# Optimization experiments

Measured on AMD Instinct MI355X. Metric: run time of the kernel, lower is better.

## Reference

```python
import jax, jax.numpy as jnp
import numpy as np

N = 100000   # nodes
E = 1600000  # edges
D = 128      # input = hidden channels
L = 4        # 1 + num_convs GIN layers
G = 512      # graphs in batch
BN_EPS = 1e-5


def setup_inputs() -> dict:
    key = jax.random.key(0)
    ks = jax.random.split(key, 10)
    s = 1.0 / np.sqrt(D)
    x = jax.random.normal(ks[0], (N, D), jnp.float32)
    edge_index = jax.random.randint(ks[1], (2, E), 0, N)
    batch = jnp.sort(jax.random.randint(ks[2], (N,), 0, G))
    return {
        "x": x,
        "edge_index": edge_index,
        "batch": batch,
        "W1": jax.random.normal(ks[3], (L, D, D), jnp.float32) * s,
        "b1": jnp.zeros((L, D), jnp.float32),
        "gamma": jnp.ones((L, D), jnp.float32),
        "beta": jnp.zeros((L, D), jnp.float32),
        "W2": jax.random.normal(ks[4], (L, D, D), jnp.float32) * s,
        "b2": jnp.zeros((L, D), jnp.float32),
        "lin_W": jax.random.normal(ks[5], (D, 2), jnp.float32) * s,
        "lin_b": jnp.zeros((2,), jnp.float32),
    }


def reference(x, edge_index, batch, W1, b1, gamma, beta, W2, b2, lin_W, lin_b):
    src, dst = edge_index[0], edge_index[1]
    h = x
    for l in range(L):
        # GINConv, eps=0: (1+eps)*x_i + sum_{j->i} x_j  (scatter-add over edges)
        agg = jax.ops.segment_sum(h[src], dst, num_segments=N)  # [N, D]
        z = h + agg
        # MLP: Linear -> BatchNorm1d (training stats) -> ELU -> Linear -> ELU
        z = z @ W1[l] + b1[l]
        mu = jnp.mean(z, axis=0)
        var = jnp.mean((z - mu) ** 2, axis=0)  # biased var, as torch BN
        z = (z - mu) * jax.lax.rsqrt(var + BN_EPS) * gamma[l] + beta[l]
        z = jax.nn.elu(z)
        h = jax.nn.elu(z @ W2[l] + b2[l])
    # global_mean_pool: per-graph segment mean
    sums = jax.ops.segment_sum(h, batch, num_segments=G)             # [G, D]
    cnt = jax.ops.segment_sum(jnp.ones((N, 1), h.dtype), batch, num_segments=G)
    pooled = sums / jnp.maximum(cnt, 1.0)
    return pooled @ lin_W + lin_b  # [G, 2]
```

## Files before the change

### kernel.cpp

```cpp
#include <hip/hip_runtime.h>
#include <cstdint>

#define D 128
#define BKT_SHIFT 8
#define BKT_CAP 5120
#define EDGES_PER_BLOCK 4096
#define NREP 8
#define LCAP 1536

typedef __attribute__((ext_vector_type(4))) float floatx4;
typedef __attribute__((ext_vector_type(4))) _Float16 half4;
typedef __attribute__((ext_vector_type(8))) _Float16 half8;

__device__ __forceinline__ float elu_f(float x) {
    return x > 0.0f ? x : __expf(x) - 1.0f;
}

__global__ __launch_bounds__(256) void bucket_scatter_kernel(
    const int* __restrict__ src, const int* __restrict__ dst,
    int* __restrict__ gcursor, int2* __restrict__ staging, int E, int NB) {
    __shared__ int lcnt[512];
    __shared__ int lbase[512];
    int t = threadIdx.x;
    lcnt[t] = 0; lcnt[t + 256] = 0;
    __syncthreads();
    int base = blockIdx.x * EDGES_PER_BLOCK;
    int s_[16], d_[16], r_[16];
#pragma unroll
    for (int i = 0; i < 16; ++i) {
        int idx = base + i * 256 + t;
        if (idx < E) {
            s_[i] = src[idx];
            d_[i] = dst[idx];
            r_[i] = atomicAdd(&lcnt[d_[i] >> BKT_SHIFT], 1);
        }
    }
    __syncthreads();
    for (int b = t; b < NB; b += 256) {
        int c = lcnt[b];
        if (c) lbase[b] = atomicAdd(&gcursor[b], c);
    }
    __syncthreads();
#pragma unroll
    for (int i = 0; i < 16; ++i) {
        int idx = base + i * 256 + t;
        if (idx < E) {
            int bkt = d_[i] >> BKT_SHIFT;
            staging[lbase[bkt] + r_[i]] = make_int2(s_[i], d_[i]);
        }
    }
}

__global__ __launch_bounds__(256) void bucket_build_kernel(
    const int2* __restrict__ staging, const int* __restrict__ gcursor,
    int* __restrict__ rowstart, int* __restrict__ rowend,
    int* __restrict__ col, int N) {
    __shared__ int hcnt[256];
    __shared__ int hoff[256];
    int t = threadIdx.x;
    int node0 = blockIdx.x << BKT_SHIFT;
    int off0 = blockIdx.x * BKT_CAP;
    int off1 = gcursor[blockIdx.x];
    hcnt[t] = 0;
    __syncthreads();
    for (int i = off0 + t; i < off1; i += 256)
        atomicAdd(&hcnt[staging[i].y - node0], 1);
    __syncthreads();
    int deg = hcnt[t];
    hoff[t] = deg;
    __syncthreads();
    for (int off = 1; off < 256; off <<= 1) {
        int u = (t >= off) ? hoff[t - off] : 0;
        __syncthreads();
        hoff[t] += u;
        __syncthreads();
    }
    int myoff = (t == 0) ? 0 : hoff[t - 1];
    __syncthreads();
    hoff[t] = myoff;
    hcnt[t] = 0;
    if (node0 + t < N) {
        rowstart[node0 + t] = off0 + myoff;
        rowend[node0 + t] = off0 + myoff + deg;
    }
    __syncthreads();
    for (int i = off0 + t; i < off1; i += 256) {
        int2 p = staging[i];
        int dl = p.y - node0;
        int pos = off0 + hoff[dl] + atomicAdd(&hcnt[dl], 1);
        col[pos] = p.x;
    }
}

__global__ __launch_bounds__(256) void prep_kernel(
    const float* __restrict__ x, _Float16* __restrict__ hhalf, int n4,
    const float* __restrict__ W1, const float* __restrict__ W2,
    _Float16* __restrict__ Wph, _Float16* __restrict__ Wpl, int wtot,
    int* __restrict__ gcursor, int NB, int nbh, int nbw) {
    int bid = blockIdx.x;
    int t = threadIdx.x;
    if (bid < nbh) {
        int i = bid * 256 + t;
        if (i >= n4) return;
        float4 v = ((const float4*)x)[i];
        half4 h = {(_Float16)v.x, (_Float16)v.y, (_Float16)v.z, (_Float16)v.w};
        ((half4*)hhalf)[i] = h;
    } else if (bid < nbh + nbw) {
        int idx = (bid - nbh) * 256 + t;
        if (idx >= wtot) return;
        int mat = idx >> 14;
        int rem = idx & 16383;
        int tile = rem >> 9;
        int lane = (rem >> 3) & 63;
        int j = rem & 7;
        int ks = tile >> 3, nt = tile & 7;
        int n = nt * 16 + (lane & 15);
        int k = ks * 32 + (lane >> 4) * 8 + j;
        int l = mat >> 1;
        const float* W = (mat & 1) ? W2 : W1;
        float v = W[(size_t)l * D * D + k * D + n];
        _Float16 h = (_Float16)v;
        _Float16 lo = (_Float16)(v - (float)h);
        Wph[idx] = h;
        Wpl[idx] = lo;
    } else {
        int i = (bid - nbh - nbw) * 256 + t;
        if (i < NB) gcursor[i] = i * BKT_CAP;
    }
}

template <bool GATHER, bool ELU_OUT, bool STATS, bool POOL, int MW>
__global__ __launch_bounds__(256, MW) void gemm_mfma(
    const _Float16* __restrict__ Hh,
    const int* __restrict__ rowstart, const int* __restrict__ rowend,
    const int* __restrict__ col,
    const _Float16* __restrict__ Z,
    const _Float16* __restrict__ Wph, const _Float16* __restrict__ Wpl,
    const float* __restrict__ bias,
    const float* __restrict__ colsum_in, const float* __restrict__ gamma,
    const float* __restrict__ beta,
    _Float16* __restrict__ outp16, float* __restrict__ colsum_out,
    const int* __restrict__ batchg, float* __restrict__ pooled, float* __restrict__ cnt,
    int N) {
    __shared__ _Float16 sA[64 * 136];
    __shared__ float bnsum[2 * D];
    __shared__ float s_sc[D];
    __shared__ float s_sh[D];
    __shared__ int lcol[LCAP];
    __shared__ int srow[65];
    const int tid = threadIdx.x;
    const int row0 = blockIdx.x * 64;

    if (STATS && tid < 2 * D) bnsum[tid] = 0.f;

    if (GATHER) {
        const int lastrow = (row0 + 63 < N) ? row0 + 63 : N - 1;
        const int eb0 = rowstart[row0];
        const int eb1 = rowend[lastrow];
        if (tid < 64) {
            int rr = row0 + tid;
            srow[tid] = (rr < N) ? rowstart[rr] : eb1;
        }
        if (tid == 64) srow[64] = eb1;
        for (int k = eb0 + tid; k < eb1 && (k - eb0) < LCAP; k += 256)
            lcol[k - eb0] = col[k];
        __syncthreads();

        const int rg = tid >> 4;
        const int q = tid & 15;
        const half8* hh8 = (const half8*)Hh;
#define LIDX(ee) ((((ee) - eb0) < LCAP) ? lcol[(ee) - eb0] : col[(ee)])
#pragma unroll
        for (int i = 0; i < 4; ++i) {
            int r = rg * 4 + i;
            int node = row0 + r;
            float a0 = 0.f, a1 = 0.f, a2 = 0.f, a3 = 0.f;
            float a4 = 0.f, a5 = 0.f, a6 = 0.f, a7 = 0.f;
            if (node < N) {
                half8 sf = hh8[(uint32_t)(node * 16 + q)];
                a0 = (float)sf[0]; a1 = (float)sf[1]; a2 = (float)sf[2]; a3 = (float)sf[3];
                a4 = (float)sf[4]; a5 = (float)sf[5]; a6 = (float)sf[6]; a7 = (float)sf[7];
                int e0 = srow[r], e1 = srow[r + 1];
                int e = e0;
                for (; e + 15 < e1; e += 16) {
                    int j0 = LIDX(e),      j1 = LIDX(e + 1),  j2 = LIDX(e + 2),  j3 = LIDX(e + 3);
                    int j4 = LIDX(e + 4),  j5 = LIDX(e + 5),  j6 = LIDX(e + 6),  j7 = LIDX(e + 7);
                    int j8 = LIDX(e + 8),  j9 = LIDX(e + 9),  jA = LIDX(e + 10), jB = LIDX(e + 11);
                    int jC = LIDX(e + 12), jD = LIDX(e + 13), jE = LIDX(e + 14), jF = LIDX(e + 15);
                    half8 v0 = hh8[(uint32_t)(j0 * 16 + q)];
                    half8 v1 = hh8[(uint32_t)(j1 * 16 + q)];
                    half8 v2 = hh8[(uint32_t)(j2 * 16 + q)];
                    half8 v3 = hh8[(uint32_t)(j3 * 16 + q)];
                    half8 v4 = hh8[(uint32_t)(j4 * 16 + q)];
                    half8 v5 = hh8[(uint32_t)(j5 * 16 + q)];
                    half8 v6 = hh8[(uint32_t)(j6 * 16 + q)];
                    half8 v7 = hh8[(uint32_t)(j7 * 16 + q)];
                    half8 v8 = hh8[(uint32_t)(j8 * 16 + q)];
                    half8 v9 = hh8[(uint32_t)(j9 * 16 + q)];
                    half8 vA = hh8[(uint32_t)(jA * 16 + q)];
                    half8 vB = hh8[(uint32_t)(jB * 16 + q)];
                    half8 vC = hh8[(uint32_t)(jC * 16 + q)];
                    half8 vD = hh8[(uint32_t)(jD * 16 + q)];
                    half8 vE = hh8[(uint32_t)(jE * 16 + q)];
                    half8 vF = hh8[(uint32_t)(jF * 16 + q)];
#pragma unroll
                    for (int c = 0; c < 8; ++c) {
                        float s = (((float)v0[c] + (float)v1[c]) + ((float)v2[c] + (float)v3[c]))
                                + (((float)v4[c] + (float)v5[c]) + ((float)v6[c] + (float)v7[c]))
                                + (((float)v8[c] + (float)v9[c]) + ((float)vA[c] + (float)vB[c]))
                                + (((float)vC[c] + (float)vD[c]) + ((float)vE[c] + (float)vF[c]));
                        if (c == 0) a0 += s; else if (c == 1) a1 += s;
                        else if (c == 2) a2 += s; else if (c == 3) a3 += s;
                        else if (c == 4) a4 += s; else if (c == 5) a5 += s;
                        else if (c == 6) a6 += s; else a7 += s;
                    }
                }
                if (e + 7 < e1) {
                    int j0 = LIDX(e),     j1 = LIDX(e + 1), j2 = LIDX(e + 2), j3 = LIDX(e + 3);
                    int j4 = LIDX(e + 4), j5 = LIDX(e + 5), j6 = LIDX(e + 6), j7 = LIDX(e + 7);
                    half8 v0 = hh8[(uint32_t)(j0 * 16 + q)];
                    half8 v1 = hh8[(uint32_t)(j1 * 16 + q)];
                    half8 v2 = hh8[(uint32_t)(j2 * 16 + q)];
                    half8 v3 = hh8[(uint32_t)(j3 * 16 + q)];
                    half8 v4 = hh8[(uint32_t)(j4 * 16 + q)];
                    half8 v5 = hh8[(uint32_t)(j5 * 16 + q)];
                    half8 v6 = hh8[(uint32_t)(j6 * 16 + q)];
                    half8 v7 = hh8[(uint32_t)(j7 * 16 + q)];
                    a0 += (((float)v0[0] + (float)v1[0]) + ((float)v2[0] + (float)v3[0]))
                        + (((float)v4[0] + (float)v5[0]) + ((float)v6[0] + (float)v7[0]));
                    a1 += (((float)v0[1] + (float)v1[1]) + ((float)v2[1] + (float)v3[1]))
                        + (((float)v4[1] + (float)v5[1]) + ((float)v6[1] + (float)v7[1]));
                    a2 += (((float)v0[2] + (float)v1[2]) + ((float)v2[2] + (float)v3[2]))
                        + (((float)v4[2] + (float)v5[2]) + ((float)v6[2] + (float)v7[2]));
                    a3 += (((float)v0[3] + (float)v1[3]) + ((float)v2[3] + (float)v3[3]))
                        + (((float)v4[3] + (float)v5[3]) + ((float)v6[3] + (float)v7[3]));
                    a4 += (((float)v0[4] + (float)v1[4]) + ((float)v2[4] + (float)v3[4]))
                        + (((float)v4[4] + (float)v5[4]) + ((float)v6[4] + (float)v7[4]));
                    a5 += (((float)v0[5] + (float)v1[5]) + ((float)v2[5] + (float)v3[5]))
                        + (((float)v4[5] + (float)v5[5]) + ((float)v6[5] + (float)v7[5]));
                    a6 += (((float)v0[6] + (float)v1[6]) + ((float)v2[6] + (float)v3[6]))
                        + (((float)v4[6] + (float)v5[6]) + ((float)v6[6] + (float)v7[6]));
                    a7 += (((float)v0[7] + (float)v1[7]) + ((float)v2[7] + (float)v3[7]))
                        + (((float)v4[7] + (float)v5[7]) + ((float)v6[7] + (float)v7[7]));
                    e += 8;
                }
                if (e < e1) {
                    int last = e1 - 1;
                    int e0c = e,     e1c = e + 1 > last ? last : e + 1;
                    int e2c = e + 2 > last ? last : e + 2, e3c = e + 3 > last ? last : e + 3;
                    int e4c = e + 4 > last ? last : e + 4, e5c = e + 5 > last ? last : e + 5;
                    int e6c = e + 6 > last ? last : e + 6, e7c = e + 7 > last ? last : e + 7;
                    int j0 = LIDX(e0c), j1 = LIDX(e1c), j2 = LIDX(e2c), j3 = LIDX(e3c);
                    int j4 = LIDX(e4c), j5 = LIDX(e5c), j6 = LIDX(e6c), j7 = LIDX(e7c);
                    float m1 = (e + 1 <= last) ? 1.f : 0.f, m2 = (e + 2 <= last) ? 1.f : 0.f;
                    float m3 = (e + 3 <= last) ? 1.f : 0.f, m4 = (e + 4 <= last) ? 1.f : 0.f;
                    float m5 = (e + 5 <= last) ? 1.f : 0.f, m6 = (e + 6 <= last) ? 1.f : 0.f;
                    float m7 = (e + 7 <= last) ? 1.f : 0.f;
                    half8 v0 = hh8[(uint32_t)(j0 * 16 + q)];
                    half8 v1 = hh8[(uint32_t)(j1 * 16 + q)];
                    half8 v2 = hh8[(uint32_t)(j2 * 16 + q)];
                    half8 v3 = hh8[(uint32_t)(j3 * 16 + q)];
                    half8 v4 = hh8[(uint32_t)(j4 * 16 + q)];
                    half8 v5 = hh8[(uint32_t)(j5 * 16 + q)];
                    half8 v6 = hh8[(uint32_t)(j6 * 16 + q)];
                    half8 v7 = hh8[(uint32_t)(j7 * 16 + q)];
                    a0 += (float)v0[0] + m1 * (float)v1[0] + m2 * (float)v2[0] + m3 * (float)v3[0]
                        + m4 * (float)v4[0] + m5 * (float)v5[0] + m6 * (float)v6[0] + m7 * (float)v7[0];
                    a1 += (float)v0[1] + m1 * (float)v1[1] + m2 * (float)v2[1] + m3 * (float)v3[1]
                        + m4 * (float)v4[1] + m5 * (float)v5[1] + m6 * (float)v6[1] + m7 * (float)v7[1];
                    a2 += (float)v0[2] + m1 * (float)v1[2] + m2 * (float)v2[2] + m3 * (float)v3[2]
                        + m4 * (float)v4[2] + m5 * (float)v5[2] + m6 * (float)v6[2] + m7 * (float)v7[2];
                    a3 += (float)v0[3] + m1 * (float)v1[3] + m2 * (float)v2[3] + m3 * (float)v3[3]
                        + m4 * (float)v4[3] + m5 * (float)v5[3] + m6 * (float)v6[3] + m7 * (float)v7[3];
                    a4 += (float)v0[4] + m1 * (float)v1[4] + m2 * (float)v2[4] + m3 * (float)v3[4]
                        + m4 * (float)v4[4] + m5 * (float)v5[4] + m6 * (float)v6[4] + m7 * (float)v7[4];
                    a5 += (float)v0[5] + m1 * (float)v1[5] + m2 * (float)v2[5] + m3 * (float)v3[5]
                        + m4 * (float)v4[5] + m5 * (float)v5[5] + m6 * (float)v6[5] + m7 * (float)v7[5];
                    a6 += (float)v0[6] + m1 * (float)v1[6] + m2 * (float)v2[6] + m3 * (float)v3[6]
                        + m4 * (float)v4[6] + m5 * (float)v5[6] + m6 * (float)v6[6] + m7 * (float)v7[6];
                    a7 += (float)v0[7] + m1 * (float)v1[7] + m2 * (float)v2[7] + m3 * (float)v3[7]
                        + m4 * (float)v4[7] + m5 * (float)v5[7] + m6 * (float)v6[7] + m7 * (float)v7[7];
                }
            }
            half8 hv = {(_Float16)a0, (_Float16)a1, (_Float16)a2, (_Float16)a3,
                        (_Float16)a4, (_Float16)a5, (_Float16)a6, (_Float16)a7};
            *(half8*)&sA[r * 136 + q * 8] = hv;
        }
#undef LIDX
    } else {
        if (tid < D) {
            float s = 0.f, s2 = 0.f;
#pragma unroll
            for (int rp = 0; rp < NREP; ++rp) {
                s  += colsum_in[rp * 2 * D + tid];
                s2 += colsum_in[rp * 2 * D + D + tid];
            }
            float invN = 1.0f / (float)N;
            float mu = s * invN;
            float var = s2 * invN - mu * mu;
            float rs = rsqrtf(var + 1e-5f);
            float sc = gamma[tid] * rs;
            s_sc[tid] = sc;
            s_sh[tid] = beta[tid] - mu * sc;
        }
        __syncthreads();
#pragma unroll
        for (int it = 0; it < 4; ++it) {
            int idx = tid + it * 256;
            int r = idx >> 4;
            int q8 = (idx & 15) * 8;
            int gr = row0 + r;
            half8 z = {};
            if (gr < N) z = *(const half8*)&Z[(size_t)gr * D + q8];
            float v0 = elu_f((float)z[0] * s_sc[q8 + 0] + s_sh[q8 + 0]);
            float v1 = elu_f((float)z[1] * s_sc[q8 + 1] + s_sh[q8 + 1]);
            float v2 = elu_f((float)z[2] * s_sc[q8 + 2] + s_sh[q8 + 2]);
            float v3 = elu_f((float)z[3] * s_sc[q8 + 3] + s_sh[q8 + 3]);
            float v4 = elu_f((float)z[4] * s_sc[q8 + 4] + s_sh[q8 + 4]);
            float v5 = elu_f((float)z[5] * s_sc[q8 + 5] + s_sh[q8 + 5]);
            float v6 = elu_f((float)z[6] * s_sc[q8 + 6] + s_sh[q8 + 6]);
            float v7 = elu_f((float)z[7] * s_sc[q8 + 7] + s_sh[q8 + 7]);
            half8 hv = {(_Float16)v0, (_Float16)v1, (_Float16)v2, (_Float16)v3,
                        (_Float16)v4, (_Float16)v5, (_Float16)v6, (_Float16)v7};
            *(half8*)&sA[r * 136 + q8] = hv;
        }
    }
    __syncthreads();

    const int wave = tid >> 6, lane = tid & 63;
    const int wm = wave >> 1, wn = wave & 1;
    const int l15 = lane & 15, quad = lane >> 4;
    const half8* bph = (const half8*)Wph;
    const half8* bpl = (const half8*)Wpl;

    floatx4 acc[2][4];
#pragma unroll
    for (int mt = 0; mt < 2; ++mt)
#pragma unroll
        for (int nt = 0; nt < 4; ++nt)
            acc[mt][nt] = (floatx4){0.f, 0.f, 0.f, 0.f};

#pragma unroll
    for (int ks = 0; ks < 4; ++ks) {
        const int kf = ks * 32 + quad * 8;
        half8 ah[2];
#pragma unroll
        for (int mt = 0; mt < 2; ++mt)
            ah[mt] = *(const half8*)&sA[(wm * 32 + mt * 16 + l15) * 136 + kf];
#pragma unroll
        for (int nt = 0; nt < 4; ++nt) {
            int tIdx = (ks * 8 + wn * 4 + nt) * 64 + lane;
            half8 bh = bph[tIdx];
            half8 bl = bpl[tIdx];
            acc[0][nt] = __builtin_amdgcn_mfma_f32_16x16x32_f16(ah[0], bh, acc[0][nt], 0, 0, 0);
            acc[1][nt] = __builtin_amdgcn_mfma_f32_16x16x32_f16(ah[1], bh, acc[1][nt], 0, 0, 0);
            acc[0][nt] = __builtin_amdgcn_mfma_f32_16x16x32_f16(ah[0], bl, acc[0][nt], 0, 0, 0);
            acc[1][nt] = __builtin_amdgcn_mfma_f32_16x16x32_f16(ah[1], bl, acc[1][nt], 0, 0, 0);
        }
    }

    int* sbatch = (int*)s_sc;
    if (POOL) {
        if (tid < 64) {
            int rr = row0 + tid;
            sbatch[tid] = (rr < N) ? batchg[rr] : -1;
        }
        __syncthreads();
    }

#pragma unroll
    for (int nt = 0; nt < 4; ++nt) {
        int c = wn * 64 + nt * 16 + l15;
        float b = bias[c];
        float s = 0.f, s2 = 0.f;
#pragma unroll
        for (int mt = 0; mt < 2; ++mt) {
#pragma unroll
            for (int r = 0; r < 4; ++r) {
                int rl = wm * 32 + mt * 16 + quad * 4 + r;
                int gm = row0 + rl;
                float v = acc[mt][nt][r] + b;
                if (ELU_OUT) v = elu_f(v);
                if (POOL) {
                    if (gm < N) sA[rl * 136 + c] = (_Float16)v;
                } else if (gm < N) {
                    outp16[(size_t)gm * D + c] = (_Float16)v;
                    if (STATS) { s += v; s2 += v * v; }
                }
            }
        }
        if (STATS) {
            atomicAdd(&bnsum[c], s);
            atomicAdd(&bnsum[D + c], s2);
        }
    }
    if (STATS) {
        __syncthreads();
        float* rep = colsum_out + (size_t)(blockIdx.x & (NREP - 1)) * 2 * D;
        if (tid < D) {
            atomicAdd(&rep[tid], bnsum[tid]);
            atomicAdd(&rep[D + tid], bnsum[D + tid]);
        }
    }
    if (POOL) {
        __syncthreads();
        int c = tid & 127, half = tid >> 7;
        int rb = half * 32;
        int cur = -1; float pacc = 0.f; float cc = 0.f;
        for (int i = 0; i < 32; ++i) {
            int r = rb + i;
            int gm = row0 + r;
            if (gm >= N) break;
            int g = sbatch[r];
            if (g != cur) {
                if (cur >= 0) {
                    atomicAdd(&pooled[(size_t)cur * D + c], pacc);
                    if (c == 0) atomicAdd(&cnt[cur], cc);
                }
                cur = g; pacc = 0.f; cc = 0.f;
            }
            pacc += (float)sA[r * 136 + c];
            cc += 1.f;
        }
        if (cur >= 0) {
            atomicAdd(&pooled[(size_t)cur * D + c], pacc);
            if (c == 0) atomicAdd(&cnt[cur], cc);
        }
    }
}

__global__ void final_linear_kernel(const float* __restrict__ pooled,
                                    const float* __restrict__ cnt,
                                    const float* __restrict__ linW,
                                    const float* __restrict__ linb,
                                    float* __restrict__ out, int G) {
    int t = blockIdx.x * blockDim.x + threadIdx.x;
    if (t >= G * 2) return;
    int g = t >> 1, o = t & 1;
    float inv = 1.0f / fmaxf(cnt[g], 1.0f);
    float s = linb[o];
    for (int c = 0; c < D; ++c)
        s += pooled[(size_t)g * D + c] * inv * linW[c * 2 + o];
    out[t] = s;
}

extern "C" void kernel_launch(void* const* d_in, const int* in_sizes, int n_in,
                              void* d_out, int out_size, void* d_ws, size_t ws_size,
                              hipStream_t stream) {
    const float* x      = (const float*)d_in[0];
    const int*  eidx    = (const int*)d_in[1];
    const int*  batch   = (const int*)d_in[2];
    const float* W1     = (const float*)d_in[3];
    const float* b1     = (const float*)d_in[4];
    const float* gamma  = (const float*)d_in[5];
    const float* beta   = (const float*)d_in[6];
    const float* W2     = (const float*)d_in[7];
    const float* b2     = (const float*)d_in[8];
    const float* linW   = (const float*)d_in[9];
    const float* linb   = (const float*)d_in[10];
    float* out = (float*)d_out;

    const int N = in_sizes[0] / D;
    const int E = in_sizes[1] / 2;
    const int L = in_sizes[3] / (D * D);
    const int G = out_size / 2;
    const int* esrc = eidx;
    const int* edst = eidx + E;
    const int NB = (N + 255) >> 8;

    size_t off = 0;
    auto carve = [&](size_t bytes) -> void* {
        void* p = (char*)d_ws + off;
        off += (bytes + 255) & ~(size_t)255;
        return p;
    };
    const size_t ND = (size_t)N * D;
    const int WTOT = 2 * L * D * D;
    _Float16* z16   = (_Float16*)carve(ND * 2);
    _Float16* hhalf = (_Float16*)carve(ND * 2);
    _Float16* Wph = (_Float16*)carve((size_t)WTOT * 2);
    _Float16* Wpl = (_Float16*)carve((size_t)WTOT * 2);
    int* rowstart = (int*)carve((size_t)N * 4);
    int* rowend   = (int*)carve((size_t)N * 4);
    int* col      = (int*)carve((size_t)NB * BKT_CAP * 4);
    const size_t cs_bytes = ((size_t)4 * NREP * 2 * D * 4 + 255) & ~(size_t)255;
    const size_t pl_bytes = ((size_t)G * D * 4 + 255) & ~(size_t)255;
    float* colsum4 = (float*)carve((size_t)4 * NREP * 2 * D * 4);
    float* pooled  = (float*)carve((size_t)G * D * 4);
    float* cnt     = (float*)carve((size_t)G * 4);
    int* gcursor   = (int*)carve(512 * 4);
    int2* staging = (int2*)z16;
    (void)ws_size; (void)n_in;

    hipMemsetAsync(colsum4, 0, cs_bytes + pl_bytes + (size_t)G * 4, stream);

    const int EB = (E + EDGES_PER_BLOCK - 1) / EDGES_PER_BLOCK;
    const int n4 = (int)(ND / 4);
    const int nbh = (n4 + 255) / 256;
    const int nbw = (WTOT + 255) / 256;
    const int nbc = (NB + 255) / 256;
    prep_kernel<<<nbh + nbw + nbc, 256, 0, stream>>>(
        x, hhalf, n4, W1, W2, Wph, Wpl, WTOT, gcursor, NB, nbh, nbw);
    bucket_scatter_kernel<<<EB, 256, 0, stream>>>(esrc, edst, gcursor, staging, E, NB);
    bucket_build_kernel<<<NB, 256, 0, stream>>>(staging, gcursor, rowstart, rowend, col, N);

    const int gemm_grid = (N + 63) / 64;
    for (int l = 0; l < L; ++l) {
        float* colsum = colsum4 + (size_t)l * NREP * 2 * D;
        gemm_mfma<true, false, true, false, 4><<<gemm_grid, 256, 0, stream>>>(
            hhalf, rowstart, rowend, col, nullptr,
            Wph + (size_t)(l * 2) * D * D, Wpl + (size_t)(l * 2) * D * D,
            b1 + (size_t)l * D, nullptr, nullptr, nullptr, z16, colsum,
            nullptr, nullptr, nullptr, N);
        if (l < L - 1) {
            gemm_mfma<false, true, false, false, 8><<<gemm_grid, 256, 0, stream>>>(
                nullptr, nullptr, nullptr, nullptr, z16,
                Wph + (size_t)(l * 2 + 1) * D * D, Wpl + (size_t)(l * 2 + 1) * D * D,
                b2 + (size_t)l * D, colsum, gamma + (size_t)l * D, beta + (size_t)l * D,
                hhalf, nullptr, nullptr, nullptr, nullptr, N);
        } else {
            gemm_mfma<false, true, false, true, 8><<<gemm_grid, 256, 0, stream>>>(
                nullptr, nullptr, nullptr, nullptr, z16,
                Wph + (size_t)(l * 2 + 1) * D * D, Wpl + (size_t)(l * 2 + 1) * D * D,
                b2 + (size_t)l * D, colsum, gamma + (size_t)l * D, beta + (size_t)l * D,
                nullptr, nullptr, batch, pooled, cnt, N);
        }
    }

    final_linear_kernel<<<(G * 2 + 255) / 256, 256, 0, stream>>>(pooled, cnt, linW, linb, out, G);
}
```

Baseline: 588.7 us.

## Split aggregation into feature-sliced gather kernel with sliced node layout

Node features are now stored in a column-sliced layout (8 slices of 16 halves per node), and neighbor aggregation moves out of the first GEMM into a separate kernel. Each block of that kernel handles one slice for 64 rows, so each slice's working set (about 3.2 MB) is more likely to stay in cache across the random gathers. The first GEMM then reads the sliced aggregate, and the second GEMM writes sliced output. The cost is an extra kernel launch per layer, an extra write and read of the aggregate array, an eightfold reread of the column indices, and strided stores in the sliced output.

```diff
diff --git a/kernel.cpp b/kernel.cpp
--- a/kernel.cpp
+++ b/kernel.cpp
@@ -93,7 +93,7 @@
 }
 
 __global__ __launch_bounds__(256) void prep_kernel(
-    const float* __restrict__ x, _Float16* __restrict__ hhalf, int n4,
+    const float* __restrict__ x, _Float16* __restrict__ hsl, int n4, int N,
     const float* __restrict__ W1, const float* __restrict__ W2,
     _Float16* __restrict__ Wph, _Float16* __restrict__ Wpl, int wtot,
     int* __restrict__ gcursor, int NB, int nbh, int nbw) {
@@ -104,7 +104,10 @@
         if (i >= n4) return;
         float4 v = ((const float4*)x)[i];
         half4 h = {(_Float16)v.x, (_Float16)v.y, (_Float16)v.z, (_Float16)v.w};
-        ((half4*)hhalf)[i] = h;
+        int nrow = i >> 5;
+        int c4 = (i & 31) * 4;
+        int sl = c4 >> 4, cin = c4 & 15;
+        *(half4*)(hsl + ((size_t)sl * N + nrow) * 16 + cin) = h;
     } else if (bid < nbh + nbw) {
         int idx = (bid - nbh) * 256 + t;
         if (idx >= wtot) return;
@@ -129,12 +132,132 @@
     }
 }
 
-template <bool GATHER, bool ELU_OUT, bool STATS, bool POOL, int MW>
-__global__ __launch_bounds__(256, MW) void gemm_mfma(
-    const _Float16* __restrict__ Hh,
+__global__ __launch_bounds__(256) void agg_slice_kernel(
+    const _Float16* __restrict__ hsl,
     const int* __restrict__ rowstart, const int* __restrict__ rowend,
     const int* __restrict__ col,
-    const _Float16* __restrict__ Z,
+    _Float16* __restrict__ aggsl, int N) {
+    __shared__ int lcol[LCAP];
+    __shared__ int srow[65];
+    __shared__ float pf[64][2][8];
+    const int tid = threadIdx.x;
+    const int s = blockIdx.x & 7;
+    const int row0 = (blockIdx.x >> 3) * 64;
+    const int lastrow = (row0 + 63 < N) ? row0 + 63 : N - 1;
+    const int eb0 = rowstart[row0];
+    const int eb1 = rowend[lastrow];
+    if (tid < 64) {
+        int rr = row0 + tid;
+        srow[tid] = (rr < N) ? rowstart[rr] : eb1;
+    }
+    if (tid == 64) srow[64] = eb1;
+    for (int k = eb0 + tid; k < eb1 && (k - eb0) < LCAP; k += 256)
+        lcol[k - eb0] = __builtin_nontemporal_load(&col[k]);
+    __syncthreads();
+
+    const int q2 = tid & 1;
+    const int g  = (tid >> 1) & 1;
+    const int r  = tid >> 2;
+    const int node = row0 + r;
+    const _Float16* hb = hsl + (size_t)s * N * 16;
+    float a0 = 0.f, a1 = 0.f, a2 = 0.f, a3 = 0.f;
+    float a4 = 0.f, a5 = 0.f, a6 = 0.f, a7 = 0.f;
+#define LIDX(ee) ((((ee) - eb0) < LCAP) ? lcol[(ee) - eb0] : col[(ee)])
+    if (node < N) {
+        int e1 = srow[r + 1];
+        int e = srow[r] + g;
+        for (; e + 14 < e1; e += 16) {
+            int j0 = LIDX(e),      j1 = LIDX(e + 2),  j2 = LIDX(e + 4),  j3 = LIDX(e + 6);
+            int j4 = LIDX(e + 8),  j5 = LIDX(e + 10), j6 = LIDX(e + 12), j7 = LIDX(e + 14);
+            half8 v0 = *(const half8*)(hb + (uint32_t)j0 * 16 + q2 * 8);
+            half8 v1 = *(const half8*)(hb + (uint32_t)j1 * 16 + q2 * 8);
+            half8 v2 = *(const half8*)(hb + (uint32_t)j2 * 16 + q2 * 8);
+            half8 v3 = *(const half8*)(hb + (uint32_t)j3 * 16 + q2 * 8);
+            half8 v4 = *(const half8*)(hb + (uint32_t)j4 * 16 + q2 * 8);
+            half8 v5 = *(const half8*)(hb + (uint32_t)j5 * 16 + q2 * 8);
+            half8 v6 = *(const half8*)(hb + (uint32_t)j6 * 16 + q2 * 8);
+            half8 v7 = *(const half8*)(hb + (uint32_t)j7 * 16 + q2 * 8);
+            a0 += (((float)v0[0] + (float)v1[0]) + ((float)v2[0] + (float)v3[0]))
+                + (((float)v4[0] + (float)v5[0]) + ((float)v6[0] + (float)v7[0]));
+            a1 += (((float)v0[1] + (float)v1[1]) + ((float)v2[1] + (float)v3[1]))
+                + (((float)v4[1] + (float)v5[1]) + ((float)v6[1] + (float)v7[1]));
+            a2 += (((float)v0[2] + (float)v1[2]) + ((float)v2[2] + (float)v3[2]))
+                + (((float)v4[2] + (float)v5[2]) + ((float)v6[2] + (float)v7[2]));
+            a3 += (((float)v0[3] + (float)v1[3]) + ((float)v2[3] + (float)v3[3]))
+                + (((float)v4[3] + (float)v5[3]) + ((float)v6[3] + (float)v7[3]));
+            a4 += (((float)v0[4] + (float)v1[4]) + ((float)v2[4] + (float)v3[4]))
+                + (((float)v4[4] + (float)v5[4]) + ((float)v6[4] + (float)v7[4]));
+            a5 += (((float)v0[5] + (float)v1[5]) + ((float)v2[5] + (float)v3[5]))
+                + (((float)v4[5] + (float)v5[5]) + ((float)v6[5] + (float)v7[5]));
+            a6 += (((float)v0[6] + (float)v1[6]) + ((float)v2[6] + (float)v3[6]))
+                + (((float)v4[6] + (float)v5[6]) + ((float)v6[6] + (float)v7[6]));
+            a7 += (((float)v0[7] + (float)v1[7]) + ((float)v2[7] + (float)v3[7]))
+                + (((float)v4[7] + (float)v5[7]) + ((float)v6[7] + (float)v7[7]));
+        }
+        if (e < e1) {
+            int last = e1 - 1;
+            int e0c = e;
+            int e1c = e + 2  > last ? last : e + 2,  e2c = e + 4  > last ? last : e + 4;
+            int e3c = e + 6  > last ? last : e + 6,  e4c = e + 8  > last ? last : e + 8;
+            int e5c = e + 10 > last ? last : e + 10, e6c = e + 12 > last ? last : e + 12;
+            int e7c = e + 14 > last ? last : e + 14;
+            float m1 = (e + 2  <= last) ? 1.f : 0.f, m2 = (e + 4  <= last) ? 1.f : 0.f;
+            float m3 = (e + 6  <= last) ? 1.f : 0.f, m4 = (e + 8  <= last) ? 1.f : 0.f;
+            float m5 = (e + 10 <= last) ? 1.f : 0.f, m6 = (e + 12 <= last) ? 1.f : 0.f;
+            float m7 = (e + 14 <= last) ? 1.f : 0.f;
+            int j0 = LIDX(e0c), j1 = LIDX(e1c), j2 = LIDX(e2c), j3 = LIDX(e3c);
+            int j4 = LIDX(e4c), j5 = LIDX(e5c), j6 = LIDX(e6c), j7 = LIDX(e7c);
+            half8 v0 = *(const half8*)(hb + (uint32_t)j0 * 16 + q2 * 8);
+            half8 v1 = *(const half8*)(hb + (uint32_t)j1 * 16 + q2 * 8);
+            half8 v2 = *(const half8*)(hb + (uint32_t)j2 * 16 + q2 * 8);
+            half8 v3 = *(const half8*)(hb + (uint32_t)j3 * 16 + q2 * 8);
+            half8 v4 = *(const half8*)(hb + (uint32_t)j4 * 16 + q2 * 8);
+            half8 v5 = *(const half8*)(hb + (uint32_t)j5 * 16 + q2 * 8);
+            half8 v6 = *(const half8*)(hb + (uint32_t)j6 * 16 + q2 * 8);
+            half8 v7 = *(const half8*)(hb + (uint32_t)j7 * 16 + q2 * 8);
+            a0 += (float)v0[0] + m1 * (float)v1[0] + m2 * (float)v2[0] + m3 * (float)v3[0]
+                + m4 * (float)v4[0] + m5 * (float)v5[0] + m6 * (float)v6[0] + m7 * (float)v7[0];
+            a1 += (float)v0[1] + m1 * (float)v1[1] + m2 * (float)v2[1] + m3 * (float)v3[1]
+                + m4 * (float)v4[1] + m5 * (float)v5[1] + m6 * (float)v6[1] + m7 * (float)v7[1];
+            a2 += (float)v0[2] + m1 * (float)v1[2] + m2 * (float)v2[2] + m3 * (float)v3[2]
+                + m4 * (float)v4[2] + m5 * (float)v5[2] + m6 * (float)v6[2] + m7 * (float)v7[2];
+            a3 += (float)v0[3] + m1 * (float)v1[3] + m2 * (float)v2[3] + m3 * (float)v3[3]
+                + m4 * (float)v4[3] + m5 * (float)v5[3] + m6 * (float)v6[3] + m7 * (float)v7[3];
+            a4 += (float)v0[4] + m1 * (float)v1[4] + m2 * (float)v2[4] + m3 * (float)v3[4]
+                + m4 * (float)v4[4] + m5 * (float)v5[4] + m6 * (float)v6[4] + m7 * (float)v7[4];
+            a5 += (float)v0[5] + m1 * (float)v1[5] + m2 * (float)v2[5] + m3 * (float)v3[5]
+                + m4 * (float)v4[5] + m5 * (float)v5[5] + m6 * (float)v6[5] + m7 * (float)v7[5];
+            a6 += (float)v0[6] + m1 * (float)v1[6] + m2 * (float)v2[6] + m3 * (float)v3[6]
+                + m4 * (float)v4[6] + m5 * (float)v5[6] + m6 * (float)v6[6] + m7 * (float)v7[6];
+            a7 += (float)v0[7] + m1 * (float)v1[7] + m2 * (float)v2[7] + m3 * (float)v3[7]
+                + m4 * (float)v4[7] + m5 * (float)v5[7] + m6 * (float)v6[7] + m7 * (float)v7[7];
+        }
+    }
+#undef LIDX
+    if (g == 1) {
+        pf[r][q2][0] = a0; pf[r][q2][1] = a1; pf[r][q2][2] = a2; pf[r][q2][3] = a3;
+        pf[r][q2][4] = a4; pf[r][q2][5] = a5; pf[r][q2][6] = a6; pf[r][q2][7] = a7;
+    }
+    __syncthreads();
+    if (g == 0 && node < N) {
+        half8 sf = *(const half8*)(hb + (uint32_t)node * 16 + q2 * 8);
+        a0 += (float)sf[0] + pf[r][q2][0];
+        a1 += (float)sf[1] + pf[r][q2][1];
+        a2 += (float)sf[2] + pf[r][q2][2];
+        a3 += (float)sf[3] + pf[r][q2][3];
+        a4 += (float)sf[4] + pf[r][q2][4];
+        a5 += (float)sf[5] + pf[r][q2][5];
+        a6 += (float)sf[6] + pf[r][q2][6];
+        a7 += (float)sf[7] + pf[r][q2][7];
+        half8 hv = {(_Float16)a0, (_Float16)a1, (_Float16)a2, (_Float16)a3,
+                    (_Float16)a4, (_Float16)a5, (_Float16)a6, (_Float16)a7};
+        __builtin_nontemporal_store(hv, (half8*)(aggsl + ((size_t)s * N + node) * 16 + q2 * 8));
+    }
+}
+
+template <bool SLICED_IN, bool ELU_OUT, bool STATS, bool POOL, bool SLICED_OUT>
+__global__ __launch_bounds__(256, 8) void gemm_mfma(
+    const _Float16* __restrict__ Ain,
     const _Float16* __restrict__ Wph, const _Float16* __restrict__ Wpl,
     const float* __restrict__ bias,
     const float* __restrict__ colsum_in, const float* __restrict__ gamma,
@@ -146,147 +269,23 @@
     __shared__ float bnsum[2 * D];
     __shared__ float s_sc[D];
     __shared__ float s_sh[D];
-    __shared__ int lcol[LCAP];
-    __shared__ int srow[65];
     const int tid = threadIdx.x;
     const int row0 = blockIdx.x * 64;
 
     if (STATS && tid < 2 * D) bnsum[tid] = 0.f;
 
-    if (GATHER) {
-        const int lastrow = (row0 + 63 < N) ? row0 + 63 : N - 1;
-        const int eb0 = rowstart[row0];
-        const int eb1 = rowend[lastrow];
-        if (tid < 64) {
-            int rr = row0 + tid;
-            srow[tid] = (rr < N) ? rowstart[rr] : eb1;
-        }
-        if (tid == 64) srow[64] = eb1;
-        for (int k = eb0 + tid; k < eb1 && (k - eb0) < LCAP; k += 256)
-            lcol[k - eb0] = col[k];
-        __syncthreads();
-
-        const int rg = tid >> 4;
-        const int q = tid & 15;
-        const half8* hh8 = (const half8*)Hh;
-#define LIDX(ee) ((((ee) - eb0) < LCAP) ? lcol[(ee) - eb0] : col[(ee)])
-#pragma unroll
-        for (int i = 0; i < 4; ++i) {
-            int r = rg * 4 + i;
-            int node = row0 + r;
-            float a0 = 0.f, a1 = 0.f, a2 = 0.f, a3 = 0.f;
-            float a4 = 0.f, a5 = 0.f, a6 = 0.f, a7 = 0.f;
-            if (node < N) {
-                half8 sf = hh8[(uint32_t)(node * 16 + q)];
-                a0 = (float)sf[0]; a1 = (float)sf[1]; a2 = (float)sf[2]; a3 = (float)sf[3];
-                a4 = (float)sf[4]; a5 = (float)sf[5]; a6 = (float)sf[6]; a7 = (float)sf[7];
-                int e0 = srow[r], e1 = srow[r + 1];
-                int e = e0;
-                for (; e + 15 < e1; e += 16) {
-                    int j0 = LIDX(e),      j1 = LIDX(e + 1),  j2 = LIDX(e + 2),  j3 = LIDX(e + 3);
-                    int j4 = LIDX(e + 4),  j5 = LIDX(e + 5),  j6 = LIDX(e + 6),  j7 = LIDX(e + 7);
-                    int j8 = LIDX(e + 8),  j9 = LIDX(e + 9),  jA = LIDX(e + 10), jB = LIDX(e + 11);
-                    int jC = LIDX(e + 12), jD = LIDX(e + 13), jE = LIDX(e + 14), jF = LIDX(e + 15);
-                    half8 v0 = hh8[(uint32_t)(j0 * 16 + q)];
-                    half8 v1 = hh8[(uint32_t)(j1 * 16 + q)];
-                    half8 v2 = hh8[(uint32_t)(j2 * 16 + q)];
-                    half8 v3 = hh8[(uint32_t)(j3 * 16 + q)];
-                    half8 v4 = hh8[(uint32_t)(j4 * 16 + q)];
-                    half8 v5 = hh8[(uint32_t)(j5 * 16 + q)];
-                    half8 v6 = hh8[(uint32_t)(j6 * 16 + q)];
-                    half8 v7 = hh8[(uint32_t)(j7 * 16 + q)];
-                    half8 v8 = hh8[(uint32_t)(j8 * 16 + q)];
-                    half8 v9 = hh8[(uint32_t)(j9 * 16 + q)];
-                    half8 vA = hh8[(uint32_t)(jA * 16 + q)];
-                    half8 vB = hh8[(uint32_t)(jB * 16 + q)];
-                    half8 vC = hh8[(uint32_t)(jC * 16 + q)];
-                    half8 vD = hh8[(uint32_t)(jD * 16 + q)];
-                    half8 vE = hh8[(uint32_t)(jE * 16 + q)];
-                    half8 vF = hh8[(uint32_t)(jF * 16 + q)];
-#pragma unroll
-                    for (int c = 0; c < 8; ++c) {
-                        float s = (((float)v0[c] + (float)v1[c]) + ((float)v2[c] + (float)v3[c]))
-                                + (((float)v4[c] + (float)v5[c]) + ((float)v6[c] + (float)v7[c]))
-                                + (((float)v8[c] + (float)v9[c]) + ((float)vA[c] + (float)vB[c]))
-                                + (((float)vC[c] + (float)vD[c]) + ((float)vE[c] + (float)vF[c]));
-                        if (c == 0) a0 += s; else if (c == 1) a1 += s;
-                        else if (c == 2) a2 += s; else if (c == 3) a3 += s;
-                        else if (c == 4) a4 += s; else if (c == 5) a5 += s;
-                        else if (c == 6) a6 += s; else a7 += s;
-                    }
-                }
-                if (e + 7 < e1) {
-                    int j0 = LIDX(e),     j1 = LIDX(e + 1), j2 = LIDX(e + 2), j3 = LIDX(e + 3);
-                    int j4 = LIDX(e + 4), j5 = LIDX(e + 5), j6 = LIDX(e + 6), j7 = LIDX(e + 7);
-                    half8 v0 = hh8[(uint32_t)(j0 * 16 + q)];
-                    half8 v1 = hh8[(uint32_t)(j1 * 16 + q)];
-                    half8 v2 = hh8[(uint32_t)(j2 * 16 + q)];
-                    half8 v3 = hh8[(uint32_t)(j3 * 16 + q)];
-                    half8 v4 = hh8[(uint32_t)(j4 * 16 + q)];
-                    half8 v5 = hh8[(uint32_t)(j5 * 16 + q)];
-                    half8 v6 = hh8[(uint32_t)(j6 * 16 + q)];
-                    half8 v7 = hh8[(uint32_t)(j7 * 16 + q)];
-                    a0 += (((float)v0[0] + (float)v1[0]) + ((float)v2[0] + (float)v3[0]))
-                        + (((float)v4[0] + (float)v5[0]) + ((float)v6[0] + (float)v7[0]));
-                    a1 += (((float)v0[1] + (float)v1[1]) + ((float)v2[1] + (float)v3[1]))
-                        + (((float)v4[1] + (float)v5[1]) + ((float)v6[1] + (float)v7[1]));
-                    a2 += (((float)v0[2] + (float)v1[2]) + ((float)v2[2] + (float)v3[2]))
-                        + (((float)v4[2] + (float)v5[2]) + ((float)v6[2] + (float)v7[2]));
-                    a3 += (((float)v0[3] + (float)v1[3]) + ((float)v2[3] + (float)v3[3]))
-                        + (((float)v4[3] + (float)v5[3]) + ((float)v6[3] + (float)v7[3]));
-                    a4 += (((float)v0[4] + (float)v1[4]) + ((float)v2[4] + (float)v3[4]))
-                        + (((float)v4[4] + (float)v5[4]) + ((float)v6[4] + (float)v7[4]));
-                    a5 += (((float)v0[5] + (float)v1[5]) + ((float)v2[5] + (float)v3[5]))
-                        + (((float)v4[5] + (float)v5[5]) + ((float)v6[5] + (float)v7[5]));
-                    a6 += (((float)v0[6] + (float)v1[6]) + ((float)v2[6] + (float)v3[6]))
-                        + (((float)v4[6] + (float)v5[6]) + ((float)v6[6] + (float)v7[6]));
-                    a7 += (((float)v0[7] + (float)v1[7]) + ((float)v2[7] + (float)v3[7]))
-                        + (((float)v4[7] + (float)v5[7]) + ((float)v6[7] + (float)v7[7]));
-                    e += 8;
-                }
-                if (e < e1) {
-                    int last = e1 - 1;
-                    int e0c = e,     e1c = e + 1 > last ? last : e + 1;
-                    int e2c = e + 2 > last ? last : e + 2, e3c = e + 3 > last ? last : e + 3;
-                    int e4c = e + 4 > last ? last : e + 4, e5c = e + 5 > last ? last : e + 5;
-                    int e6c = e + 6 > last ? last : e + 6, e7c = e + 7 > last ? last : e + 7;
-                    int j0 = LIDX(e0c), j1 = LIDX(e1c), j2 = LIDX(e2c), j3 = LIDX(e3c);
-                    int j4 = LIDX(e4c), j5 = LIDX(e5c), j6 = LIDX(e6c), j7 = LIDX(e7c);
-                    float m1 = (e + 1 <= last) ? 1.f : 0.f, m2 = (e + 2 <= last) ? 1.f : 0.f;
-                    float m3 = (e + 3 <= last) ? 1.f : 0.f, m4 = (e + 4 <= last) ? 1.f : 0.f;
-                    float m5 = (e + 5 <= last) ? 1.f : 0.f, m6 = (e + 6 <= last) ? 1.f : 0.f;
-                    float m7 = (e + 7 <= last) ? 1.f : 0.f;
-                    half8 v0 = hh8[(uint32_t)(j0 * 16 + q)];
-                    half8 v1 = hh8[(uint32_t)(j1 * 16 + q)];
-                    half8 v2 = hh8[(uint32_t)(j2 * 16 + q)];
-                    half8 v3 = hh8[(uint32_t)(j3 * 16 + q)];
-                    half8 v4 = hh8[(uint32_t)(j4 * 16 + q)];
-                    half8 v5 = hh8[(uint32_t)(j5 * 16 + q)];
-                    half8 v6 = hh8[(uint32_t)(j6 * 16 + q)];
-                    half8 v7 = hh8[(uint32_t)(j7 * 16 + q)];
-                    a0 += (float)v0[0] + m1 * (float)v1[0] + m2 * (float)v2[0] + m3 * (float)v3[0]
-                        + m4 * (float)v4[0] + m5 * (float)v5[0] + m6 * (float)v6[0] + m7 * (float)v7[0];
-                    a1 += (float)v0[1] + m1 * (float)v1[1] + m2 * (float)v2[1] + m3 * (float)v3[1]
-                        + m4 * (float)v4[1] + m5 * (float)v5[1] + m6 * (float)v6[1] + m7 * (float)v7[1];
-                    a2 += (float)v0[2] + m1 * (float)v1[2] + m2 * (float)v2[2] + m3 * (float)v3[2]
-                        + m4 * (float)v4[2] + m5 * (float)v5[2] + m6 * (float)v6[2] + m7 * (float)v7[2];
-                    a3 += (float)v0[3] + m1 * (float)v1[3] + m2 * (float)v2[3] + m3 * (float)v3[3]
-                        + m4 * (float)v4[3] + m5 * (float)v5[3] + m6 * (float)v6[3] + m7 * (float)v7[3];
-                    a4 += (float)v0[4] + m1 * (float)v1[4] + m2 * (float)v2[4] + m3 * (float)v3[4]
-                        + m4 * (float)v4[4] + m5 * (float)v5[4] + m6 * (float)v6[4] + m7 * (float)v7[4];
-                    a5 += (float)v0[5] + m1 * (float)v1[5] + m2 * (float)v2[5] + m3 * (float)v3[5]
-                        + m4 * (float)v4[5] + m5 * (float)v5[5] + m6 * (float)v6[5] + m7 * (float)v7[5];
-                    a6 += (float)v0[6] + m1 * (float)v1[6] + m2 * (float)v2[6] + m3 * (float)v3[6]
-                        + m4 * (float)v4[6] + m5 * (float)v5[6] + m6 * (float)v6[6] + m7 * (float)v7[6];
-                    a7 += (float)v0[7] + m1 * (float)v1[7] + m2 * (float)v2[7] + m3 * (float)v3[7]
-                        + m4 * (float)v4[7] + m5 * (float)v5[7] + m6 * (float)v6[7] + m7 * (float)v7[7];
-                }
-            }
-            half8 hv = {(_Float16)a0, (_Float16)a1, (_Float16)a2, (_Float16)a3,
-                        (_Float16)a4, (_Float16)a5, (_Float16)a6, (_Float16)a7};
-            *(half8*)&sA[r * 136 + q * 8] = hv;
-        }
-#undef LIDX
+    if (SLICED_IN) {
+#pragma unroll
+        for (int it = 0; it < 4; ++it) {
+            int idx = tid + it * 256;
+            int r = idx >> 4;
+            int q = idx & 15;
+            int gr = row0 + r;
+            half8 z = {};
+            if (gr < N)
+                z = *(const half8*)(Ain + ((size_t)(q >> 1) * N + gr) * 16 + (q & 1) * 8);
+            *(half8*)&sA[r * 136 + q * 8] = z;
+        }
     } else {
         if (tid < D) {
             float s = 0.f, s2 = 0.f;
@@ -311,7 +310,7 @@
             int q8 = (idx & 15) * 8;
             int gr = row0 + r;
             half8 z = {};
-            if (gr < N) z = *(const half8*)&Z[(size_t)gr * D + q8];
+            if (gr < N) z = *(const half8*)&Ain[(size_t)gr * D + q8];
             float v0 = elu_f((float)z[0] * s_sc[q8 + 0] + s_sh[q8 + 0]);
             float v1 = elu_f((float)z[1] * s_sc[q8 + 1] + s_sh[q8 + 1]);
             float v2 = elu_f((float)z[2] * s_sc[q8 + 2] + s_sh[q8 + 2]);
@@ -384,7 +383,10 @@
                 if (POOL) {
                     if (gm < N) sA[rl * 136 + c] = (_Float16)v;
                 } else if (gm < N) {
-                    outp16[(size_t)gm * D + c] = (_Float16)v;
+                    if (SLICED_OUT)
+                        outp16[((size_t)(c >> 4) * N + gm) * 16 + (c & 15)] = (_Float16)v;
+                    else
+                        outp16[(size_t)gm * D + c] = (_Float16)v;
                     if (STATS) { s += v; s2 += v * v; }
                 }
             }
@@ -477,7 +479,8 @@
     const size_t ND = (size_t)N * D;
     const int WTOT = 2 * L * D * D;
     _Float16* z16   = (_Float16*)carve(ND * 2);
-    _Float16* hhalf = (_Float16*)carve(ND * 2);
+    _Float16* hsl   = (_Float16*)carve(ND * 2);
+    _Float16* aggsl = (_Float16*)carve(ND * 2);
     _Float16* Wph = (_Float16*)carve((size_t)WTOT * 2);
     _Float16* Wpl = (_Float16*)carve((size_t)WTOT * 2);
     int* rowstart = (int*)carve((size_t)N * 4);
@@ -500,27 +503,28 @@
     const int nbw = (WTOT + 255) / 256;
     const int nbc = (NB + 255) / 256;
     prep_kernel<<<nbh + nbw + nbc, 256, 0, stream>>>(
-        x, hhalf, n4, W1, W2, Wph, Wpl, WTOT, gcursor, NB, nbh, nbw);
+        x, hsl, n4, N, W1, W2, Wph, Wpl, WTOT, gcursor, NB, nbh, nbw);
     bucket_scatter_kernel<<<EB, 256, 0, stream>>>(esrc, edst, gcursor, staging, E, NB);
     bucket_build_kernel<<<NB, 256, 0, stream>>>(staging, gcursor, rowstart, rowend, col, N);
 
-    const int gemm_grid = (N + 63) / 64;
+    const int RT = (N + 63) / 64;
     for (int l = 0; l < L; ++l) {
         float* colsum = colsum4 + (size_t)l * NREP * 2 * D;
-        gemm_mfma<true, false, true, false, 4><<<gemm_grid, 256, 0, stream>>>(
-            hhalf, rowstart, rowend, col, nullptr,
+        agg_slice_kernel<<<RT * 8, 256, 0, stream>>>(hsl, rowstart, rowend, col, aggsl, N);
+        gemm_mfma<true, false, true, false, false><<<RT, 256, 0, stream>>>(
+            aggsl,
             Wph + (size_t)(l * 2) * D * D, Wpl + (size_t)(l * 2) * D * D,
             b1 + (size_t)l * D, nullptr, nullptr, nullptr, z16, colsum,
             nullptr, nullptr, nullptr, N);
         if (l < L - 1) {
-            gemm_mfma<false, true, false, false, 8><<<gemm_grid, 256, 0, stream>>>(
-                nullptr, nullptr, nullptr, nullptr, z16,
+            gemm_mfma<false, true, false, false, true><<<RT, 256, 0, stream>>>(
+                z16,
                 Wph + (size_t)(l * 2 + 1) * D * D, Wpl + (size_t)(l * 2 + 1) * D * D,
                 b2 + (size_t)l * D, colsum, gamma + (size_t)l * D, beta + (size_t)l * D,
-                hhalf, nullptr, nullptr, nullptr, nullptr, N);
+                hsl, nullptr, nullptr, nullptr, nullptr, N);
         } else {
-            gemm_mfma<false, true, false, true, 8><<<gemm_grid, 256, 0, stream>>>(
-                nullptr, nullptr, nullptr, nullptr, z16,
+            gemm_mfma<false, true, false, true, false><<<RT, 256, 0, stream>>>(
+                z16,
                 Wph + (size_t)(l * 2 + 1) * D * D, Wpl + (size_t)(l * 2 + 1) * D * D,
                 b2 + (size_t)l * D, colsum, gamma + (size_t)l * D, beta + (size_t)l * D,
                 nullptr, nullptr, batch, pooled, cnt, N);
```

After: 743.5 us. 1.26x slower.
